# Performance work log

Hardware: AMD Instinct MI355X
Metric: run time of the kernel (lower is better)

The kernel has to match this reference:

```python
import jax, jax.numpy as jnp
import numpy as np

N = 100000
E = 1250000
D = 64
G = 256  # num graphs
OUT = 2
BN_EPS = 1e-5


def setup_inputs() -> dict:
    key = jax.random.key(0)
    ks = jax.random.split(key, 32)
    def lin(k, fi, fo):
        return jax.random.normal(k, (fi, fo), jnp.float32) / np.sqrt(fi)
    inp = {
        "x": jax.random.normal(ks[0], (N, D), jnp.float32),
        "edge_index": jax.random.randint(ks[1], (2, E), 0, N, jnp.int32),
        "batch": jnp.sort(jax.random.randint(ks[2], (N,), 0, G, jnp.int32)),
        "w0a": lin(ks[3], D, D), "b0a": jax.random.normal(ks[4], (D,)) * 0.02,
        "w0b": lin(ks[5], D, D), "b0b": jax.random.normal(ks[6], (D,)) * 0.02,
        "w1a": lin(ks[7], D, D), "b1a": jax.random.normal(ks[8], (D,)) * 0.02,
        "w1b": lin(ks[9], D, D), "b1b": jax.random.normal(ks[10], (D,)) * 0.02,
        "w2a": lin(ks[11], D, D), "b2a": jax.random.normal(ks[12], (D,)) * 0.02,
        "w2b": lin(ks[13], D, D), "b2b": jax.random.normal(ks[14], (D,)) * 0.02,
        "bn0_g": jax.random.uniform(ks[15], (D,), minval=0.5, maxval=1.5),
        "bn0_b": jax.random.normal(ks[16], (D,)) * 0.02,
        "bn0_m": jax.random.normal(ks[17], (D,)) * 0.1,
        "bn0_v": jax.random.uniform(ks[18], (D,), minval=0.5, maxval=1.5),
        "bn1_g": jax.random.uniform(ks[19], (D,), minval=0.5, maxval=1.5),
        "bn1_b": jax.random.normal(ks[20], (D,)) * 0.02,
        "bn1_m": jax.random.normal(ks[21], (D,)) * 0.1,
        "bn1_v": jax.random.uniform(ks[22], (D,), minval=0.5, maxval=1.5),
        "wp1": lin(ks[23], 2 * D, D), "bp1": jax.random.normal(ks[24], (D,)) * 0.02,
        "wp2": lin(ks[25], D, OUT), "bp2": jax.random.normal(ks[26], (OUT,)) * 0.02,
    }
    return inp


def _gin(x, edge_index, wa, ba, wb, bb):
    # GINConv (eps=0): MLP(x + sum_{j->i} x_j); messages flow src->dst
    agg = jax.ops.segment_sum(x[edge_index[0]], edge_index[1], num_segments=N)
    h = x + agg
    h = jnp.maximum(h @ wa + ba, 0.0) @ wb + bb
    return h


def _bn(x, g, b, m, v):
    return (x - m) * (g * jax.lax.rsqrt(v + BN_EPS)) + b


def reference(x, edge_index, batch,
              w0a, b0a, w0b, b0b, w1a, b1a, w1b, b1b, w2a, b2a, w2b, b2b,
              bn0_g, bn0_b, bn0_m, bn0_v, bn1_g, bn1_b, bn1_m, bn1_v,
              wp1, bp1, wp2, bp2):
    # eval mode: dropout = identity, BatchNorm uses running stats
    h = jnp.maximum(_gin(x, edge_index, w0a, b0a, w0b, b0b), 0.0)
    h = _bn(h, bn0_g, bn0_b, bn0_m, bn0_v)
    h = jnp.maximum(_gin(h, edge_index, w1a, b1a, w1b, b1b), 0.0)
    h = _bn(h, bn1_g, bn1_b, bn1_m, bn1_v)
    h = jnp.maximum(_gin(h, edge_index, w2a, b2a, w2b, b2b), 0.0)
    # global mean + max pool over graphs
    counts = jax.ops.segment_sum(jnp.ones((N,), h.dtype), batch, num_segments=G)
    mean = jax.ops.segment_sum(h, batch, num_segments=G) / jnp.maximum(counts, 1.0)[:, None]
    mx = jax.ops.segment_max(h, batch, num_segments=G)
    mx = jnp.where(jnp.isfinite(mx), mx, 0.0)  # guard empty graphs
    graph_x = jnp.concatenate([mean, mx], axis=1)  # [G, 2D]
    pred = (graph_x @ wp1 + bp1) @ wp2 + bp2
    return jax.nn.log_softmax(pred, axis=1)
```

## Files before the change

kernel.cpp:

```cpp
#include <hip/hip_runtime.h>
#include <hip/hip_bf16.h>

#define NN 100000
#define EE 1250000
#define DD 64
#define GG 256
#define COARSE 1024
#define NC ((NN + COARSE - 1) / COARSE)
#define CHUNK 2048
#define NCHUNK ((EE + CHUNK - 1) / CHUNK)

static __device__ __forceinline__ float relu_f(float x) { return fmaxf(x, 0.0f); }

static __device__ __forceinline__ float b2f(ushort u) {
    return __uint_as_float(((unsigned int)u) << 16);
}
static __device__ __forceinline__ ushort f2b(float f) {
    __hip_bfloat16 h = __float2bfloat16(f);
    return *(ushort*)&h;
}

__global__ __launch_bounds__(256) void hist2_kernel(const int* __restrict__ dst,
                                                    int* __restrict__ ghist, int E) {
    __shared__ int h[NC];
    int t = threadIdx.x;
    if (t < NC) h[t] = 0;
    __syncthreads();
    for (int e = blockIdx.x * blockDim.x + t; e < E; e += gridDim.x * blockDim.x)
        atomicAdd(&h[dst[e] >> 10], 1);
    __syncthreads();
    if (t < NC && h[t]) atomicAdd(&ghist[t], h[t]);
}

__global__ void scan2_kernel(const int* __restrict__ ghist, int* __restrict__ coffs,
                             int* __restrict__ gcursor) {
    if (threadIdx.x == 0) {
        int run = 0;
        for (int b = 0; b < NC; b++) {
            coffs[b] = run;
            gcursor[b] = run;
            run += ghist[b];
        }
        coffs[NC] = run;
    }
}

__global__ __launch_bounds__(256) void bin_kernel(
    const int* __restrict__ ei, int* __restrict__ gcursor, int* __restrict__ epack, int E) {
    __shared__ int hist[NC];
    __shared__ int base[NC];
    __shared__ int lpre[NC];
    __shared__ int scnt;
    __shared__ int lbuf[CHUNK];
    __shared__ int lobuf[CHUNK];
    int t = threadIdx.x;
    for (int c = blockIdx.x; c < NCHUNK; c += gridDim.x) {
        int e0 = c * CHUNK;
        if (t < NC) hist[t] = 0;
        __syncthreads();
        int myb[8], myloc[8], mypack[8];
#pragma unroll
        for (int q = 0; q < 8; q++) {
            int e = e0 + q * 256 + t;
            if (e < E) {
                int d = ei[E + e];
                int s = ei[e];
                int b = d >> 10;
                myb[q] = b;
                mypack[q] = s | ((d & (COARSE - 1)) << 17);
                myloc[q] = atomicAdd(&hist[b], 1);
            } else myb[q] = -1;
        }
        __syncthreads();
        if (t < NC) base[t] = hist[t] ? atomicAdd(&gcursor[t], hist[t]) : 0;
        if (t == 0) {
            int run = 0;
            for (int b = 0; b < NC; b++) { lpre[b] = run; run += hist[b]; }
            scnt = run;
        }
        __syncthreads();
#pragma unroll
        for (int q = 0; q < 8; q++) {
            if (myb[q] >= 0) {
                int p = lpre[myb[q]] + myloc[q];
                lbuf[p] = mypack[q];
                lobuf[p] = base[myb[q]] + myloc[q];
            }
        }
        __syncthreads();
        int cnt = scnt;
#pragma unroll
        for (int q = 0; q < 8; q++) {
            int p = q * 256 + t;
            if (p < cnt) epack[lobuf[p]] = lbuf[p];
        }
        __syncthreads();
    }
}

__global__ __launch_bounds__(256) void csr2_kernel(
    const int* __restrict__ epack, const int* __restrict__ coffs,
    int* __restrict__ srcs, int* __restrict__ off) {
    __shared__ int hist[COARSE];
    __shared__ int tmp[256];
    int b = blockIdx.x;
    int t = threadIdx.x;
    int c0 = coffs[b], c1 = coffs[b + 1];
    int nbase = b * COARSE;
#pragma unroll
    for (int j = 0; j < 4; j++) hist[t * 4 + j] = 0;
    __syncthreads();
    for (int e = c0 + t; e < c1; e += 256)
        atomicAdd(&hist[epack[e] >> 17], 1);
    __syncthreads();
    int h0 = hist[t * 4], h1 = hist[t * 4 + 1], h2 = hist[t * 4 + 2], h3 = hist[t * 4 + 3];
    int s4 = h0 + h1 + h2 + h3;
    tmp[t] = s4;
    __syncthreads();
    for (int d = 1; d < 256; d <<= 1) {
        int v = (t >= d) ? tmp[t - d] : 0;
        __syncthreads();
        tmp[t] += v;
        __syncthreads();
    }
    int run = tmp[t] - s4;
    int pre0 = run; run += h0;
    int pre1 = run; run += h1;
    int pre2 = run; run += h2;
    int pre3 = run;
    int pres[4] = {pre0, pre1, pre2, pre3};
#pragma unroll
    for (int j = 0; j < 4; j++) {
        int node = nbase + t * 4 + j;
        if (node < NN) off[node] = c0 + pres[j];
        hist[t * 4 + j] = pres[j];
    }
    if (b == NC - 1 && t == 0) off[NN] = c1;
    __syncthreads();
    for (int e = c0 + t; e < c1; e += 256) {
        int p = epack[e];
        int pos = c0 + atomicAdd(&hist[p >> 17], 1);
        srcs[pos] = p & 0x1FFFF;
    }
}

__global__ void bounds_kernel(const int* __restrict__ batch, int* __restrict__ gstart, int n) {
    int i = blockIdx.x * blockDim.x + threadIdx.x;
    if (i >= n) return;
    int b = batch[i];
    int prev = (i == 0) ? -1 : batch[i - 1];
    for (int g = prev + 1; g <= b; g++) gstart[g] = i;
    if (i == n - 1) {
        for (int g = b + 1; g <= GG; g++) gstart[g] = n;
    }
}

__global__ __launch_bounds__(256) void cast_kernel(const float* __restrict__ x,
                                                   ushort* __restrict__ xb) {
    size_t i = ((size_t)blockIdx.x * blockDim.x + threadIdx.x) * 4;
    if (i >= (size_t)NN * DD) return;
    float4 v = *(const float4*)(x + i);
    ushort4 r;
    r.x = f2b(v.x); r.y = f2b(v.y); r.z = f2b(v.z); r.w = f2b(v.w);
    *(ushort4*)(xb + i) = r;
}

__global__ __launch_bounds__(256) void agg_kernel(
    const ushort* __restrict__ xb, float* __restrict__ u,
    const int* __restrict__ off, const int* __restrict__ srcs, int n) {
    int node = blockIdx.x * 4 + (threadIdx.x >> 6);
    int lane = threadIdx.x & 63;
    if (node >= n) return;
    int o = off[node];
    int oe = off[node + 1];
    float a0 = b2f(xb[(size_t)node * DD + lane]);
    float a1 = 0.0f, a2 = 0.0f, a3 = 0.0f, a4 = 0.0f, a5 = 0.0f, a6 = 0.0f, a7 = 0.0f;
    int j = o;
    for (; j + 8 <= oe; j += 8) {
        int s0 = srcs[j + 0], s1 = srcs[j + 1], s2 = srcs[j + 2], s3 = srcs[j + 3];
        int s4 = srcs[j + 4], s5 = srcs[j + 5], s6 = srcs[j + 6], s7 = srcs[j + 7];
        ushort v0 = xb[(size_t)s0 * DD + lane];
        ushort v1 = xb[(size_t)s1 * DD + lane];
        ushort v2 = xb[(size_t)s2 * DD + lane];
        ushort v3 = xb[(size_t)s3 * DD + lane];
        ushort v4 = xb[(size_t)s4 * DD + lane];
        ushort v5 = xb[(size_t)s5 * DD + lane];
        ushort v6 = xb[(size_t)s6 * DD + lane];
        ushort v7 = xb[(size_t)s7 * DD + lane];
        a0 += b2f(v0); a1 += b2f(v1); a2 += b2f(v2); a3 += b2f(v3);
        a4 += b2f(v4); a5 += b2f(v5); a6 += b2f(v6); a7 += b2f(v7);
    }
    for (; j + 4 <= oe; j += 4) {
        int s0 = srcs[j + 0], s1 = srcs[j + 1], s2 = srcs[j + 2], s3 = srcs[j + 3];
        ushort v0 = xb[(size_t)s0 * DD + lane];
        ushort v1 = xb[(size_t)s1 * DD + lane];
        ushort v2 = xb[(size_t)s2 * DD + lane];
        ushort v3 = xb[(size_t)s3 * DD + lane];
        a0 += b2f(v0); a1 += b2f(v1); a2 += b2f(v2); a3 += b2f(v3);
    }
    for (; j < oe; j++) a0 += b2f(xb[(size_t)srcs[j] * DD + lane]);
    u[(size_t)node * DD + lane] = ((a0 + a1) + (a2 + a3)) + ((a4 + a5) + (a6 + a7));
}

template <bool HAS_BN, bool OUT_BF16>
__global__ __launch_bounds__(256) void mlp_kernel(
    const float* __restrict__ u, void* __restrict__ hout,
    const float* __restrict__ wa, const float* __restrict__ ba,
    const float* __restrict__ wb, const float* __restrict__ bb,
    const float* __restrict__ bng, const float* __restrict__ bnb,
    const float* __restrict__ bnm, const float* __restrict__ bnv, int n) {
    __shared__ float At[DD][68];
    __shared__ float Wt[DD * DD];
    int t = threadIdx.x;
    int r0 = blockIdx.x * DD;
    int tx = t & 15, ty = t >> 4;
    int i0 = tx * 4, j0 = ty * 4;

    {
        int ii = t >> 2;
        int cb = (t & 3) * 16;
        int row = r0 + ii;
        if (row < n) {
            const float4* ur = (const float4*)(u + (size_t)row * DD + cb);
            float4 v0 = ur[0], v1 = ur[1], v2 = ur[2], v3 = ur[3];
            At[cb + 0][ii] = v0.x;  At[cb + 1][ii] = v0.y;
            At[cb + 2][ii] = v0.z;  At[cb + 3][ii] = v0.w;
            At[cb + 4][ii] = v1.x;  At[cb + 5][ii] = v1.y;
            At[cb + 6][ii] = v1.z;  At[cb + 7][ii] = v1.w;
            At[cb + 8][ii] = v2.x;  At[cb + 9][ii] = v2.y;
            At[cb + 10][ii] = v2.z; At[cb + 11][ii] = v2.w;
            At[cb + 12][ii] = v3.x; At[cb + 13][ii] = v3.y;
            At[cb + 14][ii] = v3.z; At[cb + 15][ii] = v3.w;
        } else {
#pragma unroll
            for (int q = 0; q < 16; q++) At[cb + q][ii] = 0.0f;
        }
#pragma unroll
        for (int rep = 0; rep < 4; rep++) {
            int idx = rep * 1024 + t * 4;
            *(float4*)&Wt[idx] = *(const float4*)&wa[idx];
        }
    }
    __syncthreads();

    float acc[4][4];
#pragma unroll
    for (int a = 0; a < 4; a++)
#pragma unroll
        for (int b = 0; b < 4; b++) acc[a][b] = 0.0f;
#pragma unroll 4
    for (int k = 0; k < DD; k++) {
        float4 av = *(const float4*)&At[k][i0];
        float4 wv = *(const float4*)&Wt[k * DD + j0];
        float aa[4] = {av.x, av.y, av.z, av.w};
        float ww[4] = {wv.x, wv.y, wv.z, wv.w};
#pragma unroll
        for (int di = 0; di < 4; di++)
#pragma unroll
            for (int dj = 0; dj < 4; dj++)
                acc[di][dj] = fmaf(aa[di], ww[dj], acc[di][dj]);
    }
    float4 ba4 = *(const float4*)&ba[j0];
    float bav[4] = {ba4.x, ba4.y, ba4.z, ba4.w};
    __syncthreads();

#pragma unroll
    for (int dj = 0; dj < 4; dj++) {
        float4 w;
        w.x = relu_f(acc[0][dj] + bav[dj]);
        w.y = relu_f(acc[1][dj] + bav[dj]);
        w.z = relu_f(acc[2][dj] + bav[dj]);
        w.w = relu_f(acc[3][dj] + bav[dj]);
        *(float4*)&At[j0 + dj][i0] = w;
    }
#pragma unroll
    for (int rep = 0; rep < 4; rep++) {
        int idx = rep * 1024 + t * 4;
        *(float4*)&Wt[idx] = *(const float4*)&wb[idx];
    }
    __syncthreads();

    float acc2[4][4];
#pragma unroll
    for (int a = 0; a < 4; a++)
#pragma unroll
        for (int b = 0; b < 4; b++) acc2[a][b] = 0.0f;
#pragma unroll 4
    for (int k = 0; k < DD; k++) {
        float4 av = *(const float4*)&At[k][i0];
        float4 wv = *(const float4*)&Wt[k * DD + j0];
        float aa[4] = {av.x, av.y, av.z, av.w};
        float ww[4] = {wv.x, wv.y, wv.z, wv.w};
#pragma unroll
        for (int di = 0; di < 4; di++)
#pragma unroll
            for (int dj = 0; dj < 4; dj++)
                acc2[di][dj] = fmaf(aa[di], ww[dj], acc2[di][dj]);
    }

    float4 bb4 = *(const float4*)&bb[j0];
    float bbv[4] = {bb4.x, bb4.y, bb4.z, bb4.w};
    float scv[4] = {0, 0, 0, 0}, shv[4] = {0, 0, 0, 0};
    if (HAS_BN) {
        float4 g4 = *(const float4*)&bng[j0];
        float4 b4 = *(const float4*)&bnb[j0];
        float4 m4 = *(const float4*)&bnm[j0];
        float4 v4 = *(const float4*)&bnv[j0];
        float gg[4] = {g4.x, g4.y, g4.z, g4.w};
        float bbn[4] = {b4.x, b4.y, b4.z, b4.w};
        float mm[4] = {m4.x, m4.y, m4.z, m4.w};
        float vv[4] = {v4.x, v4.y, v4.z, v4.w};
#pragma unroll
        for (int c = 0; c < 4; c++) {
            scv[c] = gg[c] * rsqrtf(vv[c] + 1e-5f);
            shv[c] = bbn[c] - mm[c] * scv[c];
        }
    }
#pragma unroll
    for (int di = 0; di < 4; di++) {
        int row = r0 + i0 + di;
        if (row >= n) break;
        float v[4];
#pragma unroll
        for (int dj = 0; dj < 4; dj++) {
            float tv = relu_f(acc2[di][dj] + bbv[dj]);
            if (HAS_BN) tv = fmaf(tv, scv[dj], shv[dj]);
            v[dj] = tv;
        }
        if (OUT_BF16) {
            ushort4 r;
            r.x = f2b(v[0]); r.y = f2b(v[1]); r.z = f2b(v[2]); r.w = f2b(v[3]);
            *(ushort4*)((ushort*)hout + (size_t)row * DD + j0) = r;
        } else {
            float4 r; r.x = v[0]; r.y = v[1]; r.z = v[2]; r.w = v[3];
            *(float4*)((float*)hout + (size_t)row * DD + j0) = r;
        }
    }
}

__global__ __launch_bounds__(256) void pool_kernel(
    const float* __restrict__ h, const int* __restrict__ gstart,
    float* __restrict__ pmean, float* __restrict__ pmax) {
    __shared__ float ssum[4][DD];
    __shared__ float smax[4][DD];
    int g = blockIdx.x;
    int lane = threadIdx.x & 63;
    int wave = threadIdx.x >> 6;
    int s = gstart[g], e = gstart[g + 1];
    float sum = 0.0f, mx = 0.0f;
    for (int i = s + wave; i < e; i += 4) {
        float v = h[(size_t)i * DD + lane];
        sum += v;
        mx = fmaxf(mx, v);
    }
    ssum[wave][lane] = sum;
    smax[wave][lane] = mx;
    __syncthreads();
    if (wave == 0) {
        sum = ssum[0][lane] + ssum[1][lane] + ssum[2][lane] + ssum[3][lane];
        mx = fmaxf(fmaxf(smax[0][lane], smax[1][lane]),
                   fmaxf(smax[2][lane], smax[3][lane]));
        float cnt = fmaxf((float)(e - s), 1.0f);
        pmean[g * DD + lane] = sum / cnt;
        pmax[g * DD + lane] = mx;
    }
}

__global__ __launch_bounds__(64) void head_kernel(
    const float* __restrict__ pmean, const float* __restrict__ pmax,
    const float* __restrict__ wp1, const float* __restrict__ bp1,
    const float* __restrict__ wp2, const float* __restrict__ bp2,
    float* __restrict__ out) {
    __shared__ float gx[2 * DD];
    int g = blockIdx.x;
    int lane = threadIdx.x;
    gx[lane] = pmean[g * DD + lane];
    gx[DD + lane] = pmax[g * DD + lane];
    __syncthreads();
    float t = bp1[lane];
    for (int k = 0; k < 2 * DD; k++) t = fmaf(gx[k], wp1[k * DD + lane], t);
    float p0 = t * wp2[lane * 2 + 0];
    float p1 = t * wp2[lane * 2 + 1];
    for (int o = 32; o > 0; o >>= 1) {
        p0 += __shfl_down(p0, o);
        p1 += __shfl_down(p1, o);
    }
    if (lane == 0) {
        p0 += bp2[0];
        p1 += bp2[1];
        float m = fmaxf(p0, p1);
        float lse = m + logf(expf(p0 - m) + expf(p1 - m));
        out[g * 2 + 0] = p0 - lse;
        out[g * 2 + 1] = p1 - lse;
    }
}

extern "C" void kernel_launch(void* const* d_in, const int* in_sizes, int n_in,
                              void* d_out, int out_size, void* d_ws, size_t ws_size,
                              hipStream_t stream) {
    const float* x     = (const float*)d_in[0];
    const int*   ei    = (const int*)d_in[1];
    const int*   batch = (const int*)d_in[2];
    const float* w0a = (const float*)d_in[3];  const float* b0a = (const float*)d_in[4];
    const float* w0b = (const float*)d_in[5];  const float* b0b = (const float*)d_in[6];
    const float* w1a = (const float*)d_in[7];  const float* b1a = (const float*)d_in[8];
    const float* w1b = (const float*)d_in[9];  const float* b1b = (const float*)d_in[10];
    const float* w2a = (const float*)d_in[11]; const float* b2a = (const float*)d_in[12];
    const float* w2b = (const float*)d_in[13]; const float* b2b = (const float*)d_in[14];
    const float* bn0g = (const float*)d_in[15]; const float* bn0b = (const float*)d_in[16];
    const float* bn0m = (const float*)d_in[17]; const float* bn0v = (const float*)d_in[18];
    const float* bn1g = (const float*)d_in[19]; const float* bn1b = (const float*)d_in[20];
    const float* bn1m = (const float*)d_in[21]; const float* bn1v = (const float*)d_in[22];
    const float* wp1 = (const float*)d_in[23]; const float* bp1 = (const float*)d_in[24];
    const float* wp2 = (const float*)d_in[25]; const float* bp2 = (const float*)d_in[26];
    float* out = (float*)d_out;

    char* p = (char*)d_ws;
    auto take = [&](size_t bytes) {
        char* r = p;
        p += (bytes + 255) & ~(size_t)255;
        return r;
    };
    int* ghist   = (int*)take(NC * sizeof(int));
    int* coffs   = (int*)take((NC + 1) * sizeof(int));
    int* gcursor = (int*)take(NC * sizeof(int));
    int* epack   = (int*)take(EE * sizeof(int));
    int* srcs    = (int*)take(EE * sizeof(int));
    int* off     = (int*)take((NN + 1) * sizeof(int));
    int* gstart  = (int*)take((GG + 1) * sizeof(int));
    ushort* xb   = (ushort*)take((size_t)NN * DD * sizeof(ushort));
    float* bufU  = (float*)take((size_t)NN * DD * sizeof(float));
    ushort* hA   = (ushort*)take((size_t)NN * DD * sizeof(ushort));
    ushort* hB   = (ushort*)take((size_t)NN * DD * sizeof(ushort));
    float* hC    = (float*)take((size_t)NN * DD * sizeof(float));
    float* pmean = (float*)take(GG * DD * sizeof(float));
    float* pmax  = (float*)take(GG * DD * sizeof(float));

    hipMemsetAsync(ghist, 0, NC * sizeof(int), stream);
    hist2_kernel<<<512, 256, 0, stream>>>(ei + EE, ghist, EE);
    scan2_kernel<<<1, 64, 0, stream>>>(ghist, coffs, gcursor);
    bin_kernel<<<512, 256, 0, stream>>>(ei, gcursor, epack, EE);
    csr2_kernel<<<NC, 256, 0, stream>>>(epack, coffs, srcs, off);
    bounds_kernel<<<(NN + 255) / 256, 256, 0, stream>>>(batch, gstart, NN);
    cast_kernel<<<(NN * DD / 4 + 255) / 256, 256, 0, stream>>>(x, xb);

    int agg_grid = (NN + 3) / 4;
    int mlp_grid = (NN + DD - 1) / DD;

    agg_kernel<<<agg_grid, 256, 0, stream>>>(xb, bufU, off, srcs, NN);
    mlp_kernel<true, true><<<mlp_grid, 256, 0, stream>>>(bufU, hA, w0a, b0a, w0b, b0b,
                                                         bn0g, bn0b, bn0m, bn0v, NN);
    agg_kernel<<<agg_grid, 256, 0, stream>>>(hA, bufU, off, srcs, NN);
    mlp_kernel<true, true><<<mlp_grid, 256, 0, stream>>>(bufU, hB, w1a, b1a, w1b, b1b,
                                                         bn1g, bn1b, bn1m, bn1v, NN);
    agg_kernel<<<agg_grid, 256, 0, stream>>>(hB, bufU, off, srcs, NN);
    mlp_kernel<false, false><<<mlp_grid, 256, 0, stream>>>(bufU, hC, w2a, b2a, w2b, b2b,
                                                           nullptr, nullptr, nullptr, nullptr, NN);

    pool_kernel<<<GG, 256, 0, stream>>>(hC, gstart, pmean, pmax);
    head_kernel<<<GG, 64, 0, stream>>>(pmean, pmax, wp1, bp1, wp2, bp2, out);
}
```

Before: 342.6 us.

## Fuse neighbor aggregation into MLP kernel and merge pool with head

The gather-sum aggregation now runs inside the MLP kernel: each block's four waves aggregate 16 nodes each straight into the shared-memory A tile, so the fp32 intermediate buffer is never written to or read back from global memory. Pool and head are also merged into one kernel, which drops a launch and the pmean/pmax buffers. In exchange the aggregation runs with fewer blocks, 64 nodes per block instead of 4. Each wave handles 16 nodes one after another, which may hide gather latency less well and adds load imbalance before the barrier.

```diff
diff --git a/kernel.cpp b/kernel.cpp
--- a/kernel.cpp
+++ b/kernel.cpp
@@ -165,46 +165,10 @@
     *(ushort4*)(xb + i) = r;
 }
 
-__global__ __launch_bounds__(256) void agg_kernel(
-    const ushort* __restrict__ xb, float* __restrict__ u,
-    const int* __restrict__ off, const int* __restrict__ srcs, int n) {
-    int node = blockIdx.x * 4 + (threadIdx.x >> 6);
-    int lane = threadIdx.x & 63;
-    if (node >= n) return;
-    int o = off[node];
-    int oe = off[node + 1];
-    float a0 = b2f(xb[(size_t)node * DD + lane]);
-    float a1 = 0.0f, a2 = 0.0f, a3 = 0.0f, a4 = 0.0f, a5 = 0.0f, a6 = 0.0f, a7 = 0.0f;
-    int j = o;
-    for (; j + 8 <= oe; j += 8) {
-        int s0 = srcs[j + 0], s1 = srcs[j + 1], s2 = srcs[j + 2], s3 = srcs[j + 3];
-        int s4 = srcs[j + 4], s5 = srcs[j + 5], s6 = srcs[j + 6], s7 = srcs[j + 7];
-        ushort v0 = xb[(size_t)s0 * DD + lane];
-        ushort v1 = xb[(size_t)s1 * DD + lane];
-        ushort v2 = xb[(size_t)s2 * DD + lane];
-        ushort v3 = xb[(size_t)s3 * DD + lane];
-        ushort v4 = xb[(size_t)s4 * DD + lane];
-        ushort v5 = xb[(size_t)s5 * DD + lane];
-        ushort v6 = xb[(size_t)s6 * DD + lane];
-        ushort v7 = xb[(size_t)s7 * DD + lane];
-        a0 += b2f(v0); a1 += b2f(v1); a2 += b2f(v2); a3 += b2f(v3);
-        a4 += b2f(v4); a5 += b2f(v5); a6 += b2f(v6); a7 += b2f(v7);
-    }
-    for (; j + 4 <= oe; j += 4) {
-        int s0 = srcs[j + 0], s1 = srcs[j + 1], s2 = srcs[j + 2], s3 = srcs[j + 3];
-        ushort v0 = xb[(size_t)s0 * DD + lane];
-        ushort v1 = xb[(size_t)s1 * DD + lane];
-        ushort v2 = xb[(size_t)s2 * DD + lane];
-        ushort v3 = xb[(size_t)s3 * DD + lane];
-        a0 += b2f(v0); a1 += b2f(v1); a2 += b2f(v2); a3 += b2f(v3);
-    }
-    for (; j < oe; j++) a0 += b2f(xb[(size_t)srcs[j] * DD + lane]);
-    u[(size_t)node * DD + lane] = ((a0 + a1) + (a2 + a3)) + ((a4 + a5) + (a6 + a7));
-}
-
 template <bool HAS_BN, bool OUT_BF16>
-__global__ __launch_bounds__(256) void mlp_kernel(
-    const float* __restrict__ u, void* __restrict__ hout,
+__global__ __launch_bounds__(256) void fused_kernel(
+    const ushort* __restrict__ xin, void* __restrict__ hout,
+    const int* __restrict__ off, const int* __restrict__ srcs,
     const float* __restrict__ wa, const float* __restrict__ ba,
     const float* __restrict__ wb, const float* __restrict__ bb,
     const float* __restrict__ bng, const float* __restrict__ bnb,
@@ -213,35 +177,54 @@
     __shared__ float Wt[DD * DD];
     int t = threadIdx.x;
     int r0 = blockIdx.x * DD;
+    int wave = t >> 6, lane = t & 63;
+
+#pragma unroll
+    for (int rep = 0; rep < 4; rep++) {
+        int idx = rep * 1024 + t * 4;
+        *(float4*)&Wt[idx] = *(const float4*)&wa[idx];
+    }
+
+    for (int q = 0; q < 16; q++) {
+        int i = wave * 16 + q;
+        int node = r0 + i;
+        if (node < n) {
+            int o = off[node], oe = off[node + 1];
+            float a0 = b2f(xin[(size_t)node * DD + lane]);
+            float a1 = 0.0f, a2 = 0.0f, a3 = 0.0f, a4 = 0.0f, a5 = 0.0f, a6 = 0.0f, a7 = 0.0f;
+            int j = o;
+            for (; j + 8 <= oe; j += 8) {
+                int s0 = srcs[j + 0], s1 = srcs[j + 1], s2 = srcs[j + 2], s3 = srcs[j + 3];
+                int s4 = srcs[j + 4], s5 = srcs[j + 5], s6 = srcs[j + 6], s7 = srcs[j + 7];
+                ushort v0 = xin[(size_t)s0 * DD + lane];
+                ushort v1 = xin[(size_t)s1 * DD + lane];
+                ushort v2 = xin[(size_t)s2 * DD + lane];
+                ushort v3 = xin[(size_t)s3 * DD + lane];
+                ushort v4 = xin[(size_t)s4 * DD + lane];
+                ushort v5 = xin[(size_t)s5 * DD + lane];
+                ushort v6 = xin[(size_t)s6 * DD + lane];
+                ushort v7 = xin[(size_t)s7 * DD + lane];
+                a0 += b2f(v0); a1 += b2f(v1); a2 += b2f(v2); a3 += b2f(v3);
+                a4 += b2f(v4); a5 += b2f(v5); a6 += b2f(v6); a7 += b2f(v7);
+            }
+            for (; j + 4 <= oe; j += 4) {
+                int s0 = srcs[j + 0], s1 = srcs[j + 1], s2 = srcs[j + 2], s3 = srcs[j + 3];
+                ushort v0 = xin[(size_t)s0 * DD + lane];
+                ushort v1 = xin[(size_t)s1 * DD + lane];
+                ushort v2 = xin[(size_t)s2 * DD + lane];
+                ushort v3 = xin[(size_t)s3 * DD + lane];
+                a0 += b2f(v0); a1 += b2f(v1); a2 += b2f(v2); a3 += b2f(v3);
+            }
+            for (; j < oe; j++) a0 += b2f(xin[(size_t)srcs[j] * DD + lane]);
+            At[lane][i] = ((a0 + a1) + (a2 + a3)) + ((a4 + a5) + (a6 + a7));
+        } else {
+            At[lane][i] = 0.0f;
+        }
+    }
+    __syncthreads();
+
     int tx = t & 15, ty = t >> 4;
     int i0 = tx * 4, j0 = ty * 4;
-
-    {
-        int ii = t >> 2;
-        int cb = (t & 3) * 16;
-        int row = r0 + ii;
-        if (row < n) {
-            const float4* ur = (const float4*)(u + (size_t)row * DD + cb);
-            float4 v0 = ur[0], v1 = ur[1], v2 = ur[2], v3 = ur[3];
-            At[cb + 0][ii] = v0.x;  At[cb + 1][ii] = v0.y;
-            At[cb + 2][ii] = v0.z;  At[cb + 3][ii] = v0.w;
-            At[cb + 4][ii] = v1.x;  At[cb + 5][ii] = v1.y;
-            At[cb + 6][ii] = v1.z;  At[cb + 7][ii] = v1.w;
-            At[cb + 8][ii] = v2.x;  At[cb + 9][ii] = v2.y;
-            At[cb + 10][ii] = v2.z; At[cb + 11][ii] = v2.w;
-            At[cb + 12][ii] = v3.x; At[cb + 13][ii] = v3.y;
-            At[cb + 14][ii] = v3.z; At[cb + 15][ii] = v3.w;
-        } else {
-#pragma unroll
-            for (int q = 0; q < 16; q++) At[cb + q][ii] = 0.0f;
-        }
-#pragma unroll
-        for (int rep = 0; rep < 4; rep++) {
-            int idx = rep * 1024 + t * 4;
-            *(float4*)&Wt[idx] = *(const float4*)&wa[idx];
-        }
-    }
-    __syncthreads();
 
     float acc[4][4];
 #pragma unroll
@@ -338,11 +321,14 @@
     }
 }
 
-__global__ __launch_bounds__(256) void pool_kernel(
+__global__ __launch_bounds__(256) void poolhead_kernel(
     const float* __restrict__ h, const int* __restrict__ gstart,
-    float* __restrict__ pmean, float* __restrict__ pmax) {
+    const float* __restrict__ wp1, const float* __restrict__ bp1,
+    const float* __restrict__ wp2, const float* __restrict__ bp2,
+    float* __restrict__ out) {
     __shared__ float ssum[4][DD];
     __shared__ float smax[4][DD];
+    __shared__ float gx[2 * DD];
     int g = blockIdx.x;
     int lane = threadIdx.x & 63;
     int wave = threadIdx.x >> 6;
@@ -361,37 +347,27 @@
         mx = fmaxf(fmaxf(smax[0][lane], smax[1][lane]),
                    fmaxf(smax[2][lane], smax[3][lane]));
         float cnt = fmaxf((float)(e - s), 1.0f);
-        pmean[g * DD + lane] = sum / cnt;
-        pmax[g * DD + lane] = mx;
-    }
-}
-
-__global__ __launch_bounds__(64) void head_kernel(
-    const float* __restrict__ pmean, const float* __restrict__ pmax,
-    const float* __restrict__ wp1, const float* __restrict__ bp1,
-    const float* __restrict__ wp2, const float* __restrict__ bp2,
-    float* __restrict__ out) {
-    __shared__ float gx[2 * DD];
-    int g = blockIdx.x;
-    int lane = threadIdx.x;
-    gx[lane] = pmean[g * DD + lane];
-    gx[DD + lane] = pmax[g * DD + lane];
-    __syncthreads();
-    float t = bp1[lane];
-    for (int k = 0; k < 2 * DD; k++) t = fmaf(gx[k], wp1[k * DD + lane], t);
-    float p0 = t * wp2[lane * 2 + 0];
-    float p1 = t * wp2[lane * 2 + 1];
-    for (int o = 32; o > 0; o >>= 1) {
-        p0 += __shfl_down(p0, o);
-        p1 += __shfl_down(p1, o);
-    }
-    if (lane == 0) {
-        p0 += bp2[0];
-        p1 += bp2[1];
-        float m = fmaxf(p0, p1);
-        float lse = m + logf(expf(p0 - m) + expf(p1 - m));
-        out[g * 2 + 0] = p0 - lse;
-        out[g * 2 + 1] = p1 - lse;
+        gx[lane] = sum / cnt;
+        gx[DD + lane] = mx;
+    }
+    __syncthreads();
+    if (wave == 0) {
+        float tt = bp1[lane];
+        for (int k = 0; k < 2 * DD; k++) tt = fmaf(gx[k], wp1[k * DD + lane], tt);
+        float p0 = tt * wp2[lane * 2 + 0];
+        float p1 = tt * wp2[lane * 2 + 1];
+        for (int o = 32; o > 0; o >>= 1) {
+            p0 += __shfl_down(p0, o);
+            p1 += __shfl_down(p1, o);
+        }
+        if (lane == 0) {
+            p0 += bp2[0];
+            p1 += bp2[1];
+            float m = fmaxf(p0, p1);
+            float lse = m + logf(expf(p0 - m) + expf(p1 - m));
+            out[g * 2 + 0] = p0 - lse;
+            out[g * 2 + 1] = p1 - lse;
+        }
     }
 }
 
@@ -429,12 +405,9 @@
     int* off     = (int*)take((NN + 1) * sizeof(int));
     int* gstart  = (int*)take((GG + 1) * sizeof(int));
     ushort* xb   = (ushort*)take((size_t)NN * DD * sizeof(ushort));
-    float* bufU  = (float*)take((size_t)NN * DD * sizeof(float));
     ushort* hA   = (ushort*)take((size_t)NN * DD * sizeof(ushort));
     ushort* hB   = (ushort*)take((size_t)NN * DD * sizeof(ushort));
     float* hC    = (float*)take((size_t)NN * DD * sizeof(float));
-    float* pmean = (float*)take(GG * DD * sizeof(float));
-    float* pmax  = (float*)take(GG * DD * sizeof(float));
 
     hipMemsetAsync(ghist, 0, NC * sizeof(int), stream);
     hist2_kernel<<<512, 256, 0, stream>>>(ei + EE, ghist, EE);
@@ -444,19 +417,14 @@
     bounds_kernel<<<(NN + 255) / 256, 256, 0, stream>>>(batch, gstart, NN);
     cast_kernel<<<(NN * DD / 4 + 255) / 256, 256, 0, stream>>>(x, xb);
 
-    int agg_grid = (NN + 3) / 4;
-    int mlp_grid = (NN + DD - 1) / DD;
-
-    agg_kernel<<<agg_grid, 256, 0, stream>>>(xb, bufU, off, srcs, NN);
-    mlp_kernel<true, true><<<mlp_grid, 256, 0, stream>>>(bufU, hA, w0a, b0a, w0b, b0b,
-                                                         bn0g, bn0b, bn0m, bn0v, NN);
-    agg_kernel<<<agg_grid, 256, 0, stream>>>(hA, bufU, off, srcs, NN);
-    mlp_kernel<true, true><<<mlp_grid, 256, 0, stream>>>(bufU, hB, w1a, b1a, w1b, b1b,
-                                                         bn1g, bn1b, bn1m, bn1v, NN);
-    agg_kernel<<<agg_grid, 256, 0, stream>>>(hB, bufU, off, srcs, NN);
-    mlp_kernel<false, false><<<mlp_grid, 256, 0, stream>>>(bufU, hC, w2a, b2a, w2b, b2b,
-                                                           nullptr, nullptr, nullptr, nullptr, NN);
-
-    pool_kernel<<<GG, 256, 0, stream>>>(hC, gstart, pmean, pmax);
-    head_kernel<<<GG, 64, 0, stream>>>(pmean, pmax, wp1, bp1, wp2, bp2, out);
-}
+    int fuse_grid = (NN + DD - 1) / DD;
+
+    fused_kernel<true, true><<<fuse_grid, 256, 0, stream>>>(
+        xb, hA, off, srcs, w0a, b0a, w0b, b0b, bn0g, bn0b, bn0m, bn0v, NN);
+    fused_kernel<true, true><<<fuse_grid, 256, 0, stream>>>(
+        hA, hB, off, srcs, w1a, b1a, w1b, b1b, bn1g, bn1b, bn1m, bn1v, NN);
+    fused_kernel<false, false><<<fuse_grid, 256, 0, stream>>>(
+        hB, hC, off, srcs, w2a, b2a, w2b, b2b, nullptr, nullptr, nullptr, nullptr, NN);
+
+    poolhead_kernel<<<GG, 256, 0, stream>>>(hC, gstart, wp1, bp1, wp2, bp2, out);
+}
```

Result: slower. 433.0 us (+26.4%).
